# Kernel tuning notes

Measured on AMD Instinct MI355X. Metric: run time of the kernel, lower is better.

The kernel has to match this reference:

```python
import jax, jax.numpy as jnp
import numpy as np

BITS = 4
PACK = 32 // BITS  # 8 nibbles per int32
GROUP = 128
MASK = (1 << BITS) - 1


def _dequant(qweight, qzeros, scales):
    # qweight: [K//8, N] int32, nibbles packed along K (input) dim
    # qzeros : [G, N//8] int32, nibbles packed along N (output) dim
    # scales : [G, N] float
    shifts = jnp.arange(PACK, dtype=jnp.int32) * BITS  # [8]
    Kp, N = qweight.shape
    G = scales.shape[0]
    # unpack weights along input dim -> [K, N]
    w = (qweight[:, None, :] >> shifts[None, :, None]) & MASK  # [K//8, 8, N]
    w = w.reshape(Kp * PACK, N).astype(scales.dtype)
    # unpack zeros along output dim -> [G, N]
    z = (qzeros[:, :, None] >> shifts[None, None, :]) & MASK  # [G, N//8, 8]
    z = z.reshape(G, N).astype(scales.dtype) + 1.0  # GPTQ +1 zero offset
    # broadcast per-group zero/scale over GROUP consecutive input rows
    z_full = jnp.repeat(z, GROUP, axis=0)       # [K, N]
    s_full = jnp.repeat(scales, GROUP, axis=0)  # [K, N]
    return (w - z_full) * s_full  # [K, N]


def setup_inputs() -> dict:
    key = jax.random.key(0)
    k1, k2, k3, k4 = jax.random.split(key, 4)
    K, N, T = 4096, 11008, 8192
    x = jax.random.normal(k1, (T, K), dtype=jnp.float32)
    qweight = jax.random.randint(k2, (K // PACK, N), 0, 2147483647, dtype=jnp.int32)
    qzeros = jax.random.randint(k3, (K // GROUP, N // PACK), 0, 2147483647, dtype=jnp.int32)
    scales = jax.random.uniform(k4, (K // GROUP, N), dtype=jnp.float32) * 0.01
    return {"x": x, "qweight": qweight, "qzeros": qzeros, "scales": scales}


def reference(x, qweight, qzeros, scales):
    W = _dequant(qweight, qzeros, scales)  # [K, N]
    return x @ W  # [T, N]
```

## Files before the change

kernel.cpp:

```cpp
#include <hip/hip_runtime.h>
#include <hip/hip_bf16.h>
#include <cstdint>
#include <cstddef>


#define K_DIM 4096
#define N_DIM 11008
#define GROUP_SZ 128
#define KB (K_DIM * 2)
#define NTILES_K (K_DIM / 64)

typedef __bf16 bf16x8_t __attribute__((ext_vector_type(8)));
typedef float f32x4_t __attribute__((ext_vector_type(4)));

__device__ __forceinline__ void async_copy16(const void* g, void* l) {
    __builtin_amdgcn_global_load_lds((const __attribute__((address_space(1))) void*)g,
                                     (__attribute__((address_space(3))) void*)l,
                                     16, 0, 0);
}

__global__ __launch_bounds__(256) void convert_x_kernel(const float* __restrict__ x,
                                                        __bf16* __restrict__ xb,
                                                        long total) {
    long i = ((long)blockIdx.x * 256 + threadIdx.x) * 8;
    if (i >= total) return;
    const float4* p = (const float4*)(x + i);
    float4 u = p[0], v = p[1];
    bf16x8_t o;
    o[0] = (__bf16)u.x; o[1] = (__bf16)u.y; o[2] = (__bf16)u.z; o[3] = (__bf16)u.w;
    o[4] = (__bf16)v.x; o[5] = (__bf16)v.y; o[6] = (__bf16)v.z; o[7] = (__bf16)v.w;
    *(bf16x8_t*)(xb + i) = o;
}

__global__ __launch_bounds__(256) void dequant_kernel(const int* __restrict__ qw,
                                                      const int* __restrict__ qz,
                                                      const float* __restrict__ sc,
                                                      __bf16* __restrict__ Wt) {
    __shared__ __align__(16) __bf16 dqT[128 * 136];
    __shared__ float dqS[128];
    __shared__ float dqB[128];
    const int n0 = blockIdx.x * 128;
    const int g  = blockIdx.y;
    const int t  = threadIdx.x;

    if (t < 128) {
        int n = n0 + t;
        float s = sc[(size_t)g * N_DIM + n];
        int z = (qz[(size_t)g * (N_DIM / 8) + (n >> 3)] >> ((n & 7) * 4)) & 15;
        dqS[t] = s;
        dqB[t] = -(float)(z + 1) * s;
    }
    __syncthreads();

#pragma unroll
    for (int it = 0; it < 8; ++it) {
        int wi  = it * 256 + t;
        int row = wi >> 7;
        int col = wi & 127;
        int q = qw[(size_t)(g * 16 + row) * N_DIM + n0 + col];
        float s = dqS[col], b = dqB[col];
        bf16x8_t v;
#pragma unroll
        for (int j = 0; j < 8; ++j) {
            float w = (float)((q >> (4 * j)) & 15);
            v[j] = (__bf16)fmaf(w, s, b);
        }
        *(bf16x8_t*)(&dqT[col * 136 + row * 8]) = v;
    }
    __syncthreads();

    int n_loc = t & 127, half = t >> 7;
    const __bf16* src = &dqT[n_loc * 136 + half * 64];
    __bf16* dst = Wt + (size_t)(n0 + n_loc) * K_DIM + g * GROUP_SZ + half * 64;
#pragma unroll
    for (int i = 0; i < 8; ++i)
        *(bf16x8_t*)(dst + i * 8) = *(const bf16x8_t*)(src + i * 8);
}

__global__ __launch_bounds__(512, 2) void gemm256_kernel(const __bf16* __restrict__ A,
                                                         const __bf16* __restrict__ Bt,
                                                         float* __restrict__ C,
                                                         int mtiles, int ntiles) {
    __shared__ __align__(16) char ldsA[2][256 * 128];
    __shared__ __align__(16) char ldsB[2][256 * 128];
    const int tid = threadIdx.x;

    const int nwg = gridDim.x;
    const int bid = blockIdx.x;
    int vid = (nwg & 7) ? bid : ((bid & 7) * (nwg >> 3) + (bid >> 3));
    int mt, nt;
    if ((mtiles & 15) == 0) {
        const int bandsz = 16 * ntiles;
        const int band = vid / bandsz, rem = vid % bandsz;
        nt = rem >> 4;
        mt = (band << 4) + (rem & 15);
    } else {
        mt = vid % mtiles;
        nt = vid / mtiles;
    }

    const char* aPanel = (const char*)A + (size_t)mt * 256 * KB;
    const char* bPanel = (const char*)Bt + (size_t)nt * 256 * KB;

    int srcO[2], dstO[2];
#pragma unroll
    for (int q = 0; q < 2; ++q) {
        const int f = q * 512 + tid;
        const int r = f >> 3, c = f & 7;
        const int swz = (c * 16) ^ ((r & 7) << 4);
        srcO[q] = r * KB + swz;  dstO[q] = r * 128 + c * 16;
    }

    const int lane = tid & 63;
    const int wid = tid >> 6;
    const int wm = wid >> 2, wn = wid & 3;
    const int lr = lane & 15, lq = lane >> 4;
    const int kOff0 = (lq * 16) ^ ((lr & 7) << 4);
    const int kOff1 = (64 + lq * 16) ^ ((lr & 7) << 4);
    const int aRowBase = wm * 128 + lr;
    const int bRowBase = wn * 64 + lr;

    bf16x8_t aF[4][2], bF[4][2];
    f32x4_t acc[8][4];
#pragma unroll
    for (int m = 0; m < 8; ++m)
#pragma unroll
        for (int n = 0; n < 4; ++n)
            acc[m][n] = (f32x4_t){0.f, 0.f, 0.f, 0.f};

#define GL_TILE(KT, BUFS) do {                                                             \
    _Pragma("unroll") for (int h = 0; h < 2; ++h) {                                        \
        async_copy16(aPanel + (size_t)(KT) * 128 + h * 128 * KB + srcO[0],                 \
                     &ldsA[BUFS][h * 128 * 128] + dstO[0]);                                \
        async_copy16(aPanel + (size_t)(KT) * 128 + h * 128 * KB + srcO[1],                 \
                     &ldsA[BUFS][h * 128 * 128] + dstO[1]);                                \
        async_copy16(bPanel + (size_t)(KT) * 128 + h * 128 * KB + srcO[0],                 \
                     &ldsB[BUFS][h * 128 * 128] + dstO[0]);                                \
        async_copy16(bPanel + (size_t)(KT) * 128 + h * 128 * KB + srcO[1],                 \
                     &ldsB[BUFS][h * 128 * 128] + dstO[1]);                                \
    }                                                                                      \
} while (0)
#define READ_A(MQ, BUFC) do {                                                              \
    _Pragma("unroll") for (int i = 0; i < 4; ++i) {                                        \
        const char* _p = &ldsA[BUFC][(aRowBase + (MQ) * 64 + i * 16) * 128];               \
        aF[i][0] = *(const bf16x8_t*)(_p + kOff0);                                         \
        aF[i][1] = *(const bf16x8_t*)(_p + kOff1);                                         \
    }                                                                                      \
} while (0)
#define READ_B(NQ, BUFC) do {                                                              \
    _Pragma("unroll") for (int j = 0; j < 2; ++j) {                                        \
        const char* _p = &ldsB[BUFC][(bRowBase + ((NQ) * 2 + j) * 16) * 128];              \
        bF[(NQ) * 2 + j][0] = *(const bf16x8_t*)(_p + kOff0);                              \
        bF[(NQ) * 2 + j][1] = *(const bf16x8_t*)(_p + kOff1);                              \
    }                                                                                      \
} while (0)
#define MFMA_QUAD(MQ, NQ) do {                                                             \
    __builtin_amdgcn_s_setprio(1);                                                         \
    _Pragma("unroll") for (int kk = 0; kk < 2; ++kk)                                       \
    _Pragma("unroll") for (int i = 0; i < 4; ++i)                                          \
    _Pragma("unroll") for (int j = 0; j < 2; ++j)                                          \
        acc[(MQ) * 4 + i][(NQ) * 2 + j] = __builtin_amdgcn_mfma_f32_16x16x32_bf16(         \
            aF[i][kk], bF[(NQ) * 2 + j][kk], acc[(MQ) * 4 + i][(NQ) * 2 + j], 0, 0, 0);    \
    __builtin_amdgcn_s_setprio(0);                                                         \
} while (0)
#define BARRIER() asm volatile("s_barrier" ::: "memory")
#define VMCNT0()  asm volatile("s_waitcnt vmcnt(0)" ::: "memory")

#define KTILE(BUFC, KTS) do {                                                              \
    GL_TILE(KTS, (BUFC) ^ 1);                                                              \
    READ_A(0, BUFC); READ_B(0, BUFC);                                                      \
    MFMA_QUAD(0, 0);                                                                       \
    READ_B(1, BUFC);                                                                       \
    MFMA_QUAD(0, 1);                                                                       \
    READ_A(1, BUFC);                                                                       \
    MFMA_QUAD(1, 1);                                                                       \
    MFMA_QUAD(1, 0);                                                                       \
    VMCNT0(); BARRIER();                                                                   \
} while (0)

    GL_TILE(0, 0);
    VMCNT0(); BARRIER();

#pragma unroll 1
    for (int kt = 0; kt < NTILES_K; kt += 2) {
        const int ks0 = kt + 1;
        const int ks1 = (kt + 2 < NTILES_K) ? kt + 2 : kt + 1;
        KTILE(0, ks0);
        KTILE(1, ks1);
    }

#pragma unroll
    for (int m = 0; m < 8; ++m) {
        const size_t gr = (size_t)mt * 256 + wm * 128 + m * 16 + lq * 4;
#pragma unroll
        for (int n = 0; n < 4; ++n) {
            const size_t gc = (size_t)nt * 256 + wn * 64 + n * 16 + lr;
            float* cp = C + gr * N_DIM + gc;
#pragma unroll
            for (int rg = 0; rg < 4; ++rg)
                cp[(size_t)rg * N_DIM] = acc[m][n][rg];
        }
    }
}

__global__ __launch_bounds__(256) void fallback_kernel(const float* __restrict__ x,
                                                       const int* __restrict__ qw,
                                                       const int* __restrict__ qz,
                                                       const float* __restrict__ sc,
                                                       float* __restrict__ out) {
    __shared__ float xrow[K_DIM];
    const int t = blockIdx.y;
    const int n = blockIdx.x * 256 + threadIdx.x;
    for (int i = threadIdx.x; i < K_DIM; i += 256)
        xrow[i] = x[(size_t)t * K_DIM + i];
    __syncthreads();
    if (n >= N_DIM) return;
    float acc = 0.f;
    for (int g = 0; g < K_DIM / GROUP_SZ; ++g) {
        float s = sc[(size_t)g * N_DIM + n];
        int z = (qz[(size_t)g * (N_DIM / 8) + (n >> 3)] >> ((n & 7) * 4)) & 15;
        float b = -(float)(z + 1) * s;
        for (int kp = g * 16; kp < g * 16 + 16; ++kp) {
            int q = qw[(size_t)kp * N_DIM + n];
#pragma unroll
            for (int j = 0; j < 8; ++j) {
                float w = (float)((q >> (4 * j)) & 15);
                acc = fmaf(xrow[kp * 8 + j], fmaf(w, s, b), acc);
            }
        }
    }
    out[(size_t)t * N_DIM + n] = acc;
}

extern "C" void kernel_launch(void* const* d_in, const int* in_sizes, int n_in,
                              void* d_out, int out_size, void* d_ws, size_t ws_size,
                              hipStream_t stream) {
    const float* x  = (const float*)d_in[0];
    const int*   qw = (const int*)d_in[1];
    const int*   qz = (const int*)d_in[2];
    const float* sc = (const float*)d_in[3];
    float* out = (float*)d_out;

    const long T = (long)in_sizes[0] / K_DIM;
    const size_t xb_bytes = (size_t)T * K_DIM * sizeof(__bf16);
    const size_t wt_bytes = (size_t)N_DIM * K_DIM * sizeof(__bf16);

    if (ws_size >= xb_bytes + wt_bytes && (T % 256) == 0) {
        __bf16* xb = (__bf16*)d_ws;
        __bf16* Wt = (__bf16*)((char*)d_ws + xb_bytes);
        long total = T * K_DIM;
        long nthr = total / 8;
        convert_x_kernel<<<dim3((unsigned)((nthr + 255) / 256)), dim3(256), 0, stream>>>(x, xb, total);
        dequant_kernel<<<dim3(N_DIM / 128, K_DIM / GROUP_SZ), dim3(256), 0, stream>>>(qw, qz, sc, Wt);
        const int mtiles = (int)(T / 256);
        const int ntiles = N_DIM / 256;
        gemm256_kernel<<<dim3((unsigned)(mtiles * ntiles)), dim3(512), 0, stream>>>(xb, Wt, out, mtiles, ntiles);
    } else {
        fallback_kernel<<<dim3(N_DIM / 256 + 1, (unsigned)T), dim3(256), 0, stream>>>(x, qw, qz, sc, out);
    }
}
```

Measured before the change: 810.0 us.

## Interleave per-half async global-to-LDS loads with MFMA phases using partial waitcnts

Replaces the whole-tile prefetch followed by a full vmcnt(0) wait with a finer-grained schedule. A and B halves are issued separately between MFMA quads, B is prefetched a tile ahead, and the code waits with vmcnt(4) and lgkmcnt thresholds instead of draining every outstanding load. Extra barriers around each MFMA quad keep the waves in lockstep, in the style of a ping-pong schedule. The goal is to hide global memory latency behind MFMA work. In exchange it adds many more barriers and fragile buffer-reuse ordering, which risks races or added sync stalls.

```diff
diff --git a/kernel.cpp b/kernel.cpp
--- a/kernel.cpp
+++ b/kernel.cpp
@@ -128,17 +128,17 @@
         for (int n = 0; n < 4; ++n)
             acc[m][n] = (f32x4_t){0.f, 0.f, 0.f, 0.f};
 
-#define GL_TILE(KT, BUFS) do {                                                             \
-    _Pragma("unroll") for (int h = 0; h < 2; ++h) {                                        \
-        async_copy16(aPanel + (size_t)(KT) * 128 + h * 128 * KB + srcO[0],                 \
-                     &ldsA[BUFS][h * 128 * 128] + dstO[0]);                                \
-        async_copy16(aPanel + (size_t)(KT) * 128 + h * 128 * KB + srcO[1],                 \
-                     &ldsA[BUFS][h * 128 * 128] + dstO[1]);                                \
-        async_copy16(bPanel + (size_t)(KT) * 128 + h * 128 * KB + srcO[0],                 \
-                     &ldsB[BUFS][h * 128 * 128] + dstO[0]);                                \
-        async_copy16(bPanel + (size_t)(KT) * 128 + h * 128 * KB + srcO[1],                 \
-                     &ldsB[BUFS][h * 128 * 128] + dstO[1]);                                \
-    }                                                                                      \
+#define GLA(KT, BUFS, H) do {                                                              \
+    async_copy16(aPanel + (size_t)(KT) * 128 + (H) * 128 * KB + srcO[0],                   \
+                 &ldsA[BUFS][(H) * 128 * 128] + dstO[0]);                                  \
+    async_copy16(aPanel + (size_t)(KT) * 128 + (H) * 128 * KB + srcO[1],                   \
+                 &ldsA[BUFS][(H) * 128 * 128] + dstO[1]);                                  \
+} while (0)
+#define GLB(KT, BUFS, H) do {                                                              \
+    async_copy16(bPanel + (size_t)(KT) * 128 + (H) * 128 * KB + srcO[0],                   \
+                 &ldsB[BUFS][(H) * 128 * 128] + dstO[0]);                                  \
+    async_copy16(bPanel + (size_t)(KT) * 128 + (H) * 128 * KB + srcO[1],                   \
+                 &ldsB[BUFS][(H) * 128 * 128] + dstO[1]);                                  \
 } while (0)
 #define READ_A(MQ, BUFC) do {                                                              \
     _Pragma("unroll") for (int i = 0; i < 4; ++i) {                                        \
@@ -164,30 +164,64 @@
     __builtin_amdgcn_s_setprio(0);                                                         \
 } while (0)
 #define BARRIER() asm volatile("s_barrier" ::: "memory")
-#define VMCNT0()  asm volatile("s_waitcnt vmcnt(0)" ::: "memory")
-
-#define KTILE(BUFC, KTS) do {                                                              \
-    GL_TILE(KTS, (BUFC) ^ 1);                                                              \
-    READ_A(0, BUFC); READ_B(0, BUFC);                                                      \
-    MFMA_QUAD(0, 0);                                                                       \
-    READ_B(1, BUFC);                                                                       \
-    MFMA_QUAD(0, 1);                                                                       \
-    READ_A(1, BUFC);                                                                       \
-    MFMA_QUAD(1, 1);                                                                       \
-    MFMA_QUAD(1, 0);                                                                       \
-    VMCNT0(); BARRIER();                                                                   \
-} while (0)
-
-    GL_TILE(0, 0);
-    VMCNT0(); BARRIER();
+#define VMCNT4()  asm volatile("s_waitcnt vmcnt(4)" ::: "memory")
+#define LGKM0()   asm volatile("s_waitcnt lgkmcnt(0)" ::: "memory")
+#define LGKM8()   asm volatile("s_waitcnt lgkmcnt(8)" ::: "memory")
+
+    GLB(0, 0, 0); GLB(0, 0, 1); GLA(0, 0, 0); GLA(0, 0, 1);
+    GLB(1, 1, 0); GLB(1, 1, 1);
+    VMCNT4(); BARRIER();
 
 #pragma unroll 1
-    for (int kt = 0; kt < NTILES_K; kt += 2) {
-        const int ks0 = kt + 1;
-        const int ks1 = (kt + 2 < NTILES_K) ? kt + 2 : kt + 1;
-        KTILE(0, ks0);
-        KTILE(1, ks1);
-    }
+    for (int it = 0; it < NTILES_K / 2; ++it) {
+        const int b = 2 * it + 1;
+        const int c = (2 * it + 2 < NTILES_K) ? 2 * it + 2 : NTILES_K - 2;
+        const int d = (2 * it + 3 < NTILES_K) ? 2 * it + 3 : NTILES_K - 1;
+        READ_A(0, 0); READ_B(0, 0);
+        GLA(b, 1, 0);
+        LGKM8();
+        BARRIER(); LGKM0();
+        MFMA_QUAD(0, 0);
+        BARRIER();
+        READ_B(1, 0);
+        GLA(b, 1, 1);
+        BARRIER(); LGKM0();
+        MFMA_QUAD(0, 1);
+        BARRIER();
+        READ_A(1, 0);
+        GLB(c, 0, 0);
+        BARRIER(); LGKM0();
+        MFMA_QUAD(1, 1);
+        BARRIER();
+        GLB(c, 0, 1);
+        VMCNT4();
+        BARRIER();
+        MFMA_QUAD(1, 0);
+        BARRIER();
+        READ_A(0, 1); READ_B(0, 1);
+        GLA(c, 0, 0);
+        LGKM8();
+        BARRIER(); LGKM0();
+        MFMA_QUAD(0, 0);
+        BARRIER();
+        READ_B(1, 1);
+        GLA(c, 0, 1);
+        BARRIER(); LGKM0();
+        MFMA_QUAD(0, 1);
+        BARRIER();
+        READ_A(1, 1);
+        GLB(d, 1, 0);
+        BARRIER(); LGKM0();
+        MFMA_QUAD(1, 1);
+        BARRIER();
+        GLB(d, 1, 1);
+        VMCNT4();
+        BARRIER();
+        MFMA_QUAD(1, 0);
+        BARRIER();
+    }
+
+    asm volatile("s_waitcnt vmcnt(0)" ::: "memory");
 
 #pragma unroll
     for (int m = 0; m < 8; ++m) {
```

New measurement: 826.6 us. 2.1% more time.
